# Kernel tuning notes

Hardware: AMD Instinct MI355X
Metric: run time of the kernel (lower is better)

Reference implementation:

```python
import jax, jax.numpy as jnp
import numpy as np

N_NODES = 20000
N_EDGES = 320000
N_FEAT = 128
HID = 64
HEADS = 4
N_CLS = 16
NEG_SLOPE = 0.2


def setup_inputs() -> dict:
    key = jax.random.key(0)
    ks = jax.random.split(key, 12)
    x = jax.random.normal(ks[0], (N_NODES, N_FEAT), dtype=jnp.float32)
    edge_index = jax.random.randint(ks[1], (2, N_EDGES), 0, N_NODES, dtype=jnp.int64)
    # layer 1: GATConv(128 -> 64, heads=4, concat)
    s1 = 1.0 / np.sqrt(N_FEAT)
    W1 = jax.random.uniform(ks[2], (N_FEAT, HEADS * HID), jnp.float32, -s1, s1)
    a_src1 = jax.random.uniform(ks[3], (HEADS, HID), jnp.float32, -s1, s1)
    a_dst1 = jax.random.uniform(ks[4], (HEADS, HID), jnp.float32, -s1, s1)
    b1 = jnp.zeros((HEADS * HID,), jnp.float32)
    # layer 2: GATConv(256 -> 16, heads=1)
    s2 = 1.0 / np.sqrt(HEADS * HID)
    W2 = jax.random.uniform(ks[5], (HEADS * HID, N_CLS), jnp.float32, -s2, s2)
    a_src2 = jax.random.uniform(ks[6], (1, N_CLS), jnp.float32, -s2, s2)
    a_dst2 = jax.random.uniform(ks[7], (1, N_CLS), jnp.float32, -s2, s2)
    b2 = jnp.zeros((N_CLS,), jnp.float32)
    return {"x": x, "edge_index": edge_index, "W1": W1, "a_src1": a_src1,
            "a_dst1": a_dst1, "b1": b1, "W2": W2, "a_src2": a_src2,
            "a_dst2": a_dst2, "b2": b2}


def gat_conv(x, src, dst, W, a_src, a_dst, bias, n_nodes):
    # x: [N, F_in]; W: [F_in, H*C]; a_src/a_dst: [H, C]
    H, C = a_src.shape
    h = (x @ W).reshape(n_nodes, H, C)                     # [N, H, C]
    al_src = jnp.sum(h * a_src[None], axis=-1)             # [N, H]
    al_dst = jnp.sum(h * a_dst[None], axis=-1)             # [N, H]
    e = jax.nn.leaky_relu(al_src[src] + al_dst[dst], NEG_SLOPE)  # [E, H]
    # segment softmax over incoming edges of each destination node
    m = jax.ops.segment_max(e, dst, num_segments=n_nodes)  # [N, H]
    e = jnp.exp(e - m[dst])
    denom = jax.ops.segment_sum(e, dst, num_segments=n_nodes)
    alpha = e / (denom[dst] + 1e-16)                       # [E, H]
    msg = h[src] * alpha[:, :, None]                       # [E, H, C]
    out = jax.ops.segment_sum(msg, dst, num_segments=n_nodes)  # [N, H, C]
    return out.reshape(n_nodes, H * C) + bias


def reference(x, edge_index, W1, a_src1, a_dst1, b1, W2, a_src2, a_dst2, b2):
    n = x.shape[0]
    loops = jnp.arange(n, dtype=edge_index.dtype)
    src = jnp.concatenate([edge_index[0], loops])
    dst = jnp.concatenate([edge_index[1], loops])
    # eval mode: dropout is identity
    h = jax.nn.elu(gat_conv(x, src, dst, W1, a_src1, a_dst1, b1, n))
    out = gat_conv(h, src, dst, W2, a_src2, a_dst2, b2, n)
    return out
```

## Files before the change

### kernel.cpp

```cpp
#include <hip/hip_runtime.h>
#include <hip/hip_bf16.h>
#include <hip/hip_fp16.h>
#include <math.h>

#define N_NODES 20000
#define N_EDGES 320000
#define E_TOT   (N_EDGES + N_NODES)
#define N_FEAT  128
#define NEG_SLOPE 0.2f
#define MAXDEG  96

typedef _Float16 half8 __attribute__((ext_vector_type(8)));
typedef float f32x4 __attribute__((ext_vector_type(4)));

__global__ void k_init(int* __restrict__ cur,
                       const float* __restrict__ x, _Float16* __restrict__ xh,
                       const float* __restrict__ W1, _Float16* __restrict__ W1t){
  int tid = blockIdx.x * blockDim.x + threadIdx.x;
  if (tid < N_NODES) cur[tid] = 0;
  if (tid < (N_NODES * N_FEAT / 8)){
    float4 a = *(const float4*)&x[(size_t)tid * 8];
    float4 b = *(const float4*)&x[(size_t)tid * 8 + 4];
    union { __half2 h2[4]; half8 h8; } u;
    u.h2[0] = __floats2half2_rn(a.x, a.y);
    u.h2[1] = __floats2half2_rn(a.z, a.w);
    u.h2[2] = __floats2half2_rn(b.x, b.y);
    u.h2[3] = __floats2half2_rn(b.z, b.w);
    *(half8*)&xh[(size_t)tid * 8] = u.h8;
  }
  if (tid < 4096){
    int n = tid >> 4, ks = tid & 15;
    union { __half2 h2[4]; half8 h8; } u;
    float v[8];
    #pragma unroll
    for (int r = 0; r < 8; ++r) v[r] = W1[(size_t)(ks * 8 + r) * 256 + n];
    u.h2[0] = __floats2half2_rn(v[0], v[1]);
    u.h2[1] = __floats2half2_rn(v[2], v[3]);
    u.h2[2] = __floats2half2_rn(v[4], v[5]);
    u.h2[3] = __floats2half2_rn(v[6], v[7]);
    *(half8*)&W1t[(size_t)n * 128 + ks * 8] = u.h8;
  }
}

__global__ __launch_bounds__(256) void k_gemm1(
                        const _Float16* __restrict__ xh, const _Float16* __restrict__ W1t,
                        const float* __restrict__ as1, const float* __restrict__ ad1,
                        _Float16* __restrict__ h1h,
                        float* __restrict__ alS, float* __restrict__ alD,
                        const int* __restrict__ ei, int* __restrict__ cur,
                        int* __restrict__ adjS){
  __shared__ _Float16 xt[64][136];
  __shared__ _Float16 Wt[64][136];
  int t  = threadIdx.x;

  {
    int fb = blockIdx.y * 313 + blockIdx.x;
    int gtid = fb * 256 + t;
    const int GSZ = 313 * 4 * 256;
    for (int e = gtid; e < E_TOT; e += GSZ){
      int s, d;
      if (e < N_EDGES){ s = ei[e]; d = ei[N_EDGES + e]; }
      else            { s = d = e - N_EDGES; }
      int pos = atomicAdd(&cur[d], 1);
      if (pos < MAXDEG) adjS[d * MAXDEG + pos] = s;
    }
  }

  int m0 = blockIdx.x * 64;
  int by = blockIdx.y;
  int j0 = by * 64;
  #pragma unroll
  for (int ii = 0; ii < 4; ++ii){
    int f = t + ii * 256;
    int r = f >> 4, s = f & 15;
    half8 xv = (half8)(_Float16)0.f;
    if (m0 + r < N_NODES) xv = *(const half8*)&xh[(size_t)(m0 + r) * 128 + s * 8];
    *(half8*)&xt[r][s * 8] = xv;
    half8 wv = *(const half8*)&W1t[(size_t)(j0 + r) * 128 + s * 8];
    *(half8*)&Wt[r][s * 8] = wv;
  }
  __syncthreads();

  int w = t >> 6, lane = t & 63;
  int g = lane >> 4, mi = lane & 15;
  f32x4 acc[4] = {};
  #pragma unroll
  for (int kk = 0; kk < 4; ++kk){
    int ko = kk * 32 + g * 8;
    half8 b = *(const half8*)&xt[w * 16 + mi][ko];
    #pragma unroll
    for (int s = 0; s < 4; ++s){
      half8 a = *(const half8*)&Wt[s * 16 + mi][ko];
      acc[s] = __builtin_amdgcn_mfma_f32_16x16x32_f16(a, b, acc[s], 0, 0, 0);
    }
  }

  int m = m0 + w * 16 + mi;
  float s_ = 0.f, d_ = 0.f;
  #pragma unroll
  for (int s = 0; s < 4; ++s){
    int nb = j0 + s * 16 + g * 4;
    float4 asv = *(const float4*)&as1[nb];
    float4 adv = *(const float4*)&ad1[nb];
    s_ += acc[s][0] * asv.x + acc[s][1] * asv.y + acc[s][2] * asv.z + acc[s][3] * asv.w;
    d_ += acc[s][0] * adv.x + acc[s][1] * adv.y + acc[s][2] * adv.z + acc[s][3] * adv.w;
    if (m < N_NODES){
      union { __half2 h2[2]; float2 f2; } u;
      u.h2[0] = __floats2half2_rn(acc[s][0], acc[s][1]);
      u.h2[1] = __floats2half2_rn(acc[s][2], acc[s][3]);
      *(float2*)&h1h[(size_t)m * 256 + nb] = u.f2;
    }
  }
  s_ += __shfl_xor(s_, 16); s_ += __shfl_xor(s_, 32);
  d_ += __shfl_xor(d_, 16); d_ += __shfl_xor(d_, 32);
  if (g == 0 && m < N_NODES){ alS[m * 4 + by] = s_; alD[m * 4 + by] = d_; }
}

__global__ __launch_bounds__(256) void k_attn1(
                        const int* __restrict__ cur, const int* __restrict__ adjS,
                        const __half* __restrict__ h1h,
                        const float* __restrict__ alS, const float* __restrict__ alD,
                        const float* __restrict__ b1, _Float16* __restrict__ heluh){
  int b    = blockIdx.x;
  int slot = b & 7;
  int h    = slot & 3;
  int g    = (slot >> 2) * 625 + (b >> 3);
  int t    = threadIdx.x;
  int w    = t >> 6, lane = t & 63;
  int grp  = lane >> 4, l16 = lane & 15;
  int n    = g * 16 + w * 4 + grp;

  int cnt  = cur[n]; cnt = (cnt > MAXDEG) ? MAXDEG : cnt;
  int start = n * MAXDEG, end = start + cnt;
  float ald = alD[n * 4 + h];
  const __half* __restrict__ hb = h1h + h * 64 + l16 * 4;

  float4 A0 = make_float4(0.f,0.f,0.f,0.f), A1 = A0, A2 = A0, A3 = A0;
  float d0 = 0.f, d1 = 0.f, d2 = 0.f, d3 = 0.f;
  int i = start;
  if (i + 3 < end){
    int4 q = *(const int4*)&adjS[i];
    while (i + 3 < end){
      int s0 = q.x, s1 = q.y, s2 = q.z, s3 = q.w;
      int inext = i + 4;
      if (inext + 3 < end) q = *(const int4*)&adjS[inext];
      float t0 = alS[s0 * 4 + h] + ald;
      float t1 = alS[s1 * 4 + h] + ald;
      float t2 = alS[s2 * 4 + h] + ald;
      float t3 = alS[s3 * 4 + h] + ald;
      t0 = (t0 > 0.f) ? t0 : NEG_SLOPE * t0;
      t1 = (t1 > 0.f) ? t1 : NEG_SLOPE * t1;
      t2 = (t2 > 0.f) ? t2 : NEG_SLOPE * t2;
      t3 = (t3 > 0.f) ? t3 : NEG_SLOPE * t3;
      float w0 = __expf(t0), w1 = __expf(t1), w2 = __expf(t2), w3 = __expf(t3);
      float2 r0 = *(const float2*)&hb[(size_t)s0 * 256];
      float2 r1 = *(const float2*)&hb[(size_t)s1 * 256];
      float2 r2 = *(const float2*)&hb[(size_t)s2 * 256];
      float2 r3 = *(const float2*)&hb[(size_t)s3 * 256];
      const __half2* p0 = (const __half2*)&r0;
      const __half2* p1 = (const __half2*)&r1;
      const __half2* p2 = (const __half2*)&r2;
      const __half2* p3 = (const __half2*)&r3;
      float2 v0a = __half22float2(p0[0]), v0b = __half22float2(p0[1]);
      float2 v1a = __half22float2(p1[0]), v1b = __half22float2(p1[1]);
      float2 v2a = __half22float2(p2[0]), v2b = __half22float2(p2[1]);
      float2 v3a = __half22float2(p3[0]), v3b = __half22float2(p3[1]);
      A0.x += w0 * v0a.x; A0.y += w0 * v0a.y; A0.z += w0 * v0b.x; A0.w += w0 * v0b.y;
      A1.x += w1 * v1a.x; A1.y += w1 * v1a.y; A1.z += w1 * v1b.x; A1.w += w1 * v1b.y;
      A2.x += w2 * v2a.x; A2.y += w2 * v2a.y; A2.z += w2 * v2b.x; A2.w += w2 * v2b.y;
      A3.x += w3 * v3a.x; A3.y += w3 * v3a.y; A3.z += w3 * v3b.x; A3.w += w3 * v3b.y;
      d0 += w0; d1 += w1; d2 += w2; d3 += w3;
      i = inext;
    }
  }
  for (; i < end; ++i){
    int s0 = adjS[i];
    float t0 = alS[s0 * 4 + h] + ald;
    t0 = (t0 > 0.f) ? t0 : NEG_SLOPE * t0;
    float w0 = __expf(t0);
    float2 r0 = *(const float2*)&hb[(size_t)s0 * 256];
    const __half2* p0 = (const __half2*)&r0;
    float2 v0a = __half22float2(p0[0]), v0b = __half22float2(p0[1]);
    A0.x += w0 * v0a.x; A0.y += w0 * v0a.y; A0.z += w0 * v0b.x; A0.w += w0 * v0b.y;
    d0 += w0;
  }
  float rinv = 1.f / (((d0 + d1) + (d2 + d3)) + 1e-16f);
  float4 bv = *(const float4*)&b1[h * 64 + l16 * 4];
  float4 o;
  o.x = ((A0.x + A1.x) + (A2.x + A3.x)) * rinv + bv.x;
  o.y = ((A0.y + A1.y) + (A2.y + A3.y)) * rinv + bv.y;
  o.z = ((A0.z + A1.z) + (A2.z + A3.z)) * rinv + bv.z;
  o.w = ((A0.w + A1.w) + (A2.w + A3.w)) * rinv + bv.w;
  o.x = (o.x > 0.f) ? o.x : (__expf(o.x) - 1.f);
  o.y = (o.y > 0.f) ? o.y : (__expf(o.y) - 1.f);
  o.z = (o.z > 0.f) ? o.z : (__expf(o.z) - 1.f);
  o.w = (o.w > 0.f) ? o.w : (__expf(o.w) - 1.f);
  union { __half2 h2[2]; float2 f2; } u;
  u.h2[0] = __floats2half2_rn(o.x, o.y);
  u.h2[1] = __floats2half2_rn(o.z, o.w);
  *(float2*)&heluh[(size_t)n * 256 + h * 64 + l16 * 4] = u.f2;
}

__global__ __launch_bounds__(256) void k_gemm2(
                        const _Float16* __restrict__ heluh, const float* __restrict__ W2,
                        const float* __restrict__ as2, const float* __restrict__ ad2,
                        float* __restrict__ h2, float* __restrict__ alS, float* __restrict__ alD){
  __shared__ _Float16 Ht[64][264];
  __shared__ _Float16 Wt[16][264];
  int t = threadIdx.x;
  int n0 = blockIdx.x * 64;
  #pragma unroll
  for (int ii = 0; ii < 8; ++ii){
    int f = t + ii * 256;
    int r = f >> 5, s = f & 31;
    half8 v = (half8)(_Float16)0.f;
    if (n0 + r < N_NODES) v = *(const half8*)&heluh[(size_t)(n0 + r) * 256 + s * 8];
    *(half8*)&Ht[r][s * 8] = v;
  }
  {
    int k = t;
    float4 w0 = *(const float4*)&W2[k * 16 + 0];
    float4 w1 = *(const float4*)&W2[k * 16 + 4];
    float4 w2 = *(const float4*)&W2[k * 16 + 8];
    float4 w3 = *(const float4*)&W2[k * 16 + 12];
    float wv[16] = {w0.x,w0.y,w0.z,w0.w, w1.x,w1.y,w1.z,w1.w,
                    w2.x,w2.y,w2.z,w2.w, w3.x,w3.y,w3.z,w3.w};
    #pragma unroll
    for (int c = 0; c < 16; ++c) Wt[c][k] = (_Float16)wv[c];
  }
  __syncthreads();

  int w = t >> 6, lane = t & 63;
  int g = lane >> 4, mi = lane & 15;
  f32x4 acc = {};
  #pragma unroll
  for (int kk = 0; kk < 8; ++kk){
    int ko = kk * 32 + g * 8;
    half8 b = *(const half8*)&Ht[w * 16 + mi][ko];
    half8 a = *(const half8*)&Wt[mi][ko];
    acc = __builtin_amdgcn_mfma_f32_16x16x32_f16(a, b, acc, 0, 0, 0);
  }
  int n = n0 + w * 16 + mi;
  float4 asv = *(const float4*)&as2[g * 4];
  float4 adv = *(const float4*)&ad2[g * 4];
  float s_ = acc[0] * asv.x + acc[1] * asv.y + acc[2] * asv.z + acc[3] * asv.w;
  float d_ = acc[0] * adv.x + acc[1] * adv.y + acc[2] * adv.z + acc[3] * adv.w;
  s_ += __shfl_xor(s_, 16); s_ += __shfl_xor(s_, 32);
  d_ += __shfl_xor(d_, 16); d_ += __shfl_xor(d_, 32);
  if (n < N_NODES){
    float4 hv = make_float4(acc[0], acc[1], acc[2], acc[3]);
    *(float4*)&h2[(size_t)n * 16 + g * 4] = hv;
    if (g == 0){ alS[n] = s_; alD[n] = d_; }
  }
}

__global__ __launch_bounds__(256) void k_attn2(
                        const int* __restrict__ cur, const int* __restrict__ adjS,
                        const float* __restrict__ h2,
                        const float* __restrict__ alS, const float* __restrict__ alD,
                        const float* __restrict__ b2, float* __restrict__ out){
  int t    = threadIdx.x;
  int w    = t >> 6, lane = t & 63;
  int grp  = lane >> 4, l16 = lane & 15;
  int j    = l16 >> 2, c4 = l16 & 3;
  int n    = blockIdx.x * 16 + w * 4 + grp;

  int cnt  = cur[n]; cnt = (cnt > MAXDEG) ? MAXDEG : cnt;
  int start = n * MAXDEG, end = start + cnt;
  float ald = alD[n];
  float4 acc = make_float4(0.f,0.f,0.f,0.f);
  float den = 0.f;
  for (int i = start + j; i < end; i += 4){
    int s = adjS[i];
    float tt = alS[s] + ald;
    tt = (tt > 0.f) ? tt : NEG_SLOPE * tt;
    float wv = __expf(tt);
    float4 v = *(const float4*)&h2[(size_t)s * 16 + c4 * 4];
    acc.x += wv * v.x; acc.y += wv * v.y; acc.z += wv * v.z; acc.w += wv * v.w;
    den += wv;
  }
  #pragma unroll
  for (int off = 4; off <= 8; off <<= 1){
    acc.x += __shfl_xor(acc.x, off);
    acc.y += __shfl_xor(acc.y, off);
    acc.z += __shfl_xor(acc.z, off);
    acc.w += __shfl_xor(acc.w, off);
    den   += __shfl_xor(den, off);
  }
  if (j == 0){
    float rinv = 1.f / (den + 1e-16f);
    float4 bv = *(const float4*)&b2[c4 * 4];
    float4 o;
    o.x = acc.x * rinv + bv.x; o.y = acc.y * rinv + bv.y;
    o.z = acc.z * rinv + bv.z; o.w = acc.w * rinv + bv.w;
    *(float4*)&out[(size_t)n * 16 + c4 * 4] = o;
  }
}

extern "C" void kernel_launch(void* const* d_in, const int* in_sizes, int n_in,
                              void* d_out, int out_size, void* d_ws, size_t ws_size,
                              hipStream_t stream){
  const float* x   = (const float*)d_in[0];
  const int*   ei  = (const int*)d_in[1];
  const float* W1  = (const float*)d_in[2];
  const float* as1 = (const float*)d_in[3];
  const float* ad1 = (const float*)d_in[4];
  const float* b1  = (const float*)d_in[5];
  const float* W2  = (const float*)d_in[6];
  const float* as2 = (const float*)d_in[7];
  const float* ad2 = (const float*)d_in[8];
  const float* b2  = (const float*)d_in[9];
  float* out = (float*)d_out;

  float* fws = (float*)d_ws;
  size_t off = 0;
  __half* h1h = (__half*)(fws + off); off += (size_t)N_NODES * 128;
  _Float16* xh  = (_Float16*)(fws + off); off += (size_t)N_NODES * 64;
  _Float16* W1t = (_Float16*)(fws + off); off += 256 * 64;
  _Float16* heluh = (_Float16*)(fws + off); off += (size_t)N_NODES * 128;
  float* h2   = fws + off; off += (size_t)N_NODES * 16;
  float* alS1 = fws + off; off += N_NODES * 4;
  float* alD1 = fws + off; off += N_NODES * 4;
  float* alS2 = fws + off; off += N_NODES;
  float* alD2 = fws + off; off += N_NODES;
  int* cur  = (int*)(fws + off); off += N_NODES;
  int* adjS = (int*)(fws + off); off += (size_t)N_NODES * MAXDEG;

  k_init<<<(N_NODES * N_FEAT / 8 + 255) / 256, 256, 0, stream>>>(cur, x, xh, W1, W1t);
  k_gemm1<<<dim3(313, 4), 256, 0, stream>>>(xh, W1t, as1, ad1, (_Float16*)h1h,
                                            alS1, alD1, ei, cur, adjS);
  k_attn1<<<5000, 256, 0, stream>>>(cur, adjS, h1h, alS1, alD1, b1, heluh);
  k_gemm2<<<313, 256, 0, stream>>>(heluh, W2, as2, ad2, h2, alS2, alD2);
  k_attn2<<<1250, 256, 0, stream>>>(cur, adjS, h2, alS2, alD2, b2, out);
}
```

Before: 80.15 us.

## Fuse x fp16 conversion into gemm1 and split neighbor loop across half-groups

Converts x to fp16 directly while loading gemm1 tiles, removing the separate xh buffer and its write/read pass in k_init. In k_attn1, each 16-lane node group is split into two halves that process alternating quads of neighbors with 8-feature 16-byte loads, then combine partial sums via a lane shuffle. This aims to shorten the serial gather chain per lane and widen loads, at the cost of extra shuffles and half the lanes idle during the final write.

```diff
diff --git a/kernel.cpp b/kernel.cpp
--- a/kernel.cpp
+++ b/kernel.cpp
@@ -14,20 +14,9 @@
 typedef float f32x4 __attribute__((ext_vector_type(4)));
 
 __global__ void k_init(int* __restrict__ cur,
-                       const float* __restrict__ x, _Float16* __restrict__ xh,
                        const float* __restrict__ W1, _Float16* __restrict__ W1t){
   int tid = blockIdx.x * blockDim.x + threadIdx.x;
   if (tid < N_NODES) cur[tid] = 0;
-  if (tid < (N_NODES * N_FEAT / 8)){
-    float4 a = *(const float4*)&x[(size_t)tid * 8];
-    float4 b = *(const float4*)&x[(size_t)tid * 8 + 4];
-    union { __half2 h2[4]; half8 h8; } u;
-    u.h2[0] = __floats2half2_rn(a.x, a.y);
-    u.h2[1] = __floats2half2_rn(a.z, a.w);
-    u.h2[2] = __floats2half2_rn(b.x, b.y);
-    u.h2[3] = __floats2half2_rn(b.z, b.w);
-    *(half8*)&xh[(size_t)tid * 8] = u.h8;
-  }
   if (tid < 4096){
     int n = tid >> 4, ks = tid & 15;
     union { __half2 h2[4]; half8 h8; } u;
@@ -43,7 +32,7 @@
 }
 
 __global__ __launch_bounds__(256) void k_gemm1(
-                        const _Float16* __restrict__ xh, const _Float16* __restrict__ W1t,
+                        const float* __restrict__ x, const _Float16* __restrict__ W1t,
                         const float* __restrict__ as1, const float* __restrict__ ad1,
                         _Float16* __restrict__ h1h,
                         float* __restrict__ alS, float* __restrict__ alD,
@@ -74,7 +63,16 @@
     int f = t + ii * 256;
     int r = f >> 4, s = f & 15;
     half8 xv = (half8)(_Float16)0.f;
-    if (m0 + r < N_NODES) xv = *(const half8*)&xh[(size_t)(m0 + r) * 128 + s * 8];
+    if (m0 + r < N_NODES){
+      float4 a = *(const float4*)&x[(size_t)(m0 + r) * 128 + s * 8];
+      float4 bq = *(const float4*)&x[(size_t)(m0 + r) * 128 + s * 8 + 4];
+      union { __half2 h2[4]; half8 h8; } u;
+      u.h2[0] = __floats2half2_rn(a.x, a.y);
+      u.h2[1] = __floats2half2_rn(a.z, a.w);
+      u.h2[2] = __floats2half2_rn(bq.x, bq.y);
+      u.h2[3] = __floats2half2_rn(bq.z, bq.w);
+      xv = u.h8;
+    }
     *(half8*)&xt[r][s * 8] = xv;
     half8 wv = *(const half8*)&W1t[(size_t)(j0 + r) * 128 + s * 8];
     *(half8*)&Wt[r][s * 8] = wv;
@@ -128,77 +126,112 @@
   int t    = threadIdx.x;
   int w    = t >> 6, lane = t & 63;
   int grp  = lane >> 4, l16 = lane & 15;
+  int hf   = l16 >> 3, l8 = l16 & 7;
   int n    = g * 16 + w * 4 + grp;
 
   int cnt  = cur[n]; cnt = (cnt > MAXDEG) ? MAXDEG : cnt;
-  int start = n * MAXDEG, end = start + cnt;
+  int base = n * MAXDEG;
   float ald = alD[n * 4 + h];
-  const __half* __restrict__ hb = h1h + h * 64 + l16 * 4;
-
-  float4 A0 = make_float4(0.f,0.f,0.f,0.f), A1 = A0, A2 = A0, A3 = A0;
-  float d0 = 0.f, d1 = 0.f, d2 = 0.f, d3 = 0.f;
-  int i = start;
-  if (i + 3 < end){
-    int4 q = *(const int4*)&adjS[i];
-    while (i + 3 < end){
-      int s0 = q.x, s1 = q.y, s2 = q.z, s3 = q.w;
-      int inext = i + 4;
-      if (inext + 3 < end) q = *(const int4*)&adjS[inext];
+  const __half* __restrict__ hb = h1h + h * 64 + l8 * 8;
+
+  float4 Aa = make_float4(0.f,0.f,0.f,0.f), Ab = Aa;
+  float den = 0.f;
+
+  int nq = cnt >> 2;
+  for (int q = hf; q < nq; q += 2){
+    int4 quad = *(const int4*)&adjS[base + q * 4];
+    int s0 = quad.x, s1 = quad.y, s2 = quad.z, s3 = quad.w;
+    float t0 = alS[s0 * 4 + h] + ald;
+    float t1 = alS[s1 * 4 + h] + ald;
+    float t2 = alS[s2 * 4 + h] + ald;
+    float t3 = alS[s3 * 4 + h] + ald;
+    t0 = (t0 > 0.f) ? t0 : NEG_SLOPE * t0;
+    t1 = (t1 > 0.f) ? t1 : NEG_SLOPE * t1;
+    t2 = (t2 > 0.f) ? t2 : NEG_SLOPE * t2;
+    t3 = (t3 > 0.f) ? t3 : NEG_SLOPE * t3;
+    float w0 = __expf(t0), w1 = __expf(t1), w2 = __expf(t2), w3 = __expf(t3);
+    float4 r0 = *(const float4*)&hb[(size_t)s0 * 256];
+    float4 r1 = *(const float4*)&hb[(size_t)s1 * 256];
+    float4 r2 = *(const float4*)&hb[(size_t)s2 * 256];
+    float4 r3 = *(const float4*)&hb[(size_t)s3 * 256];
+    const __half2* p0 = (const __half2*)&r0;
+    const __half2* p1 = (const __half2*)&r1;
+    const __half2* p2 = (const __half2*)&r2;
+    const __half2* p3 = (const __half2*)&r3;
+    {
+      float2 a0 = __half22float2(p0[0]), a1 = __half22float2(p0[1]);
+      float2 a2 = __half22float2(p0[2]), a3 = __half22float2(p0[3]);
+      Aa.x += w0 * a0.x; Aa.y += w0 * a0.y; Aa.z += w0 * a1.x; Aa.w += w0 * a1.y;
+      Ab.x += w0 * a2.x; Ab.y += w0 * a2.y; Ab.z += w0 * a3.x; Ab.w += w0 * a3.y;
+    }
+    {
+      float2 a0 = __half22float2(p1[0]), a1 = __half22float2(p1[1]);
+      float2 a2 = __half22float2(p1[2]), a3 = __half22float2(p1[3]);
+      Aa.x += w1 * a0.x; Aa.y += w1 * a0.y; Aa.z += w1 * a1.x; Aa.w += w1 * a1.y;
+      Ab.x += w1 * a2.x; Ab.y += w1 * a2.y; Ab.z += w1 * a3.x; Ab.w += w1 * a3.y;
+    }
+    {
+      float2 a0 = __half22float2(p2[0]), a1 = __half22float2(p2[1]);
+      float2 a2 = __half22float2(p2[2]), a3 = __half22float2(p2[3]);
+      Aa.x += w2 * a0.x; Aa.y += w2 * a0.y; Aa.z += w2 * a1.x; Aa.w += w2 * a1.y;
+      Ab.x += w2 * a2.x; Ab.y += w2 * a2.y; Ab.z += w2 * a3.x; Ab.w += w2 * a3.y;
+    }
+    {
+      float2 a0 = __half22float2(p3[0]), a1 = __half22float2(p3[1]);
+      float2 a2 = __half22float2(p3[2]), a3 = __half22float2(p3[3]);
+      Aa.x += w3 * a0.x; Aa.y += w3 * a0.y; Aa.z += w3 * a1.x; Aa.w += w3 * a1.y;
+      Ab.x += w3 * a2.x; Ab.y += w3 * a2.y; Ab.z += w3 * a3.x; Ab.w += w3 * a3.y;
+    }
+    den += ((w0 + w1) + (w2 + w3));
+  }
+  if ((nq & 1) == hf){
+    for (int i = base + nq * 4; i < base + cnt; ++i){
+      int s0 = adjS[i];
       float t0 = alS[s0 * 4 + h] + ald;
-      float t1 = alS[s1 * 4 + h] + ald;
-      float t2 = alS[s2 * 4 + h] + ald;
-      float t3 = alS[s3 * 4 + h] + ald;
       t0 = (t0 > 0.f) ? t0 : NEG_SLOPE * t0;
-      t1 = (t1 > 0.f) ? t1 : NEG_SLOPE * t1;
-      t2 = (t2 > 0.f) ? t2 : NEG_SLOPE * t2;
-      t3 = (t3 > 0.f) ? t3 : NEG_SLOPE * t3;
-      float w0 = __expf(t0), w1 = __expf(t1), w2 = __expf(t2), w3 = __expf(t3);
-      float2 r0 = *(const float2*)&hb[(size_t)s0 * 256];
-      float2 r1 = *(const float2*)&hb[(size_t)s1 * 256];
-      float2 r2 = *(const float2*)&hb[(size_t)s2 * 256];
-      float2 r3 = *(const float2*)&hb[(size_t)s3 * 256];
+      float w0 = __expf(t0);
+      float4 r0 = *(const float4*)&hb[(size_t)s0 * 256];
       const __half2* p0 = (const __half2*)&r0;
-      const __half2* p1 = (const __half2*)&r1;
-      const __half2* p2 = (const __half2*)&r2;
-      const __half2* p3 = (const __half2*)&r3;
-      float2 v0a = __half22float2(p0[0]), v0b = __half22float2(p0[1]);
-      float2 v1a = __half22float2(p1[0]), v1b = __half22float2(p1[1]);
-      float2 v2a = __half22float2(p2[0]), v2b = __half22float2(p2[1]);
-      float2 v3a = __half22float2(p3[0]), v3b = __half22float2(p3[1]);
-      A0.x += w0 * v0a.x; A0.y += w0 * v0a.y; A0.z += w0 * v0b.x; A0.w += w0 * v0b.y;
-      A1.x += w1 * v1a.x; A1.y += w1 * v1a.y; A1.z += w1 * v1b.x; A1.w += w1 * v1b.y;
-      A2.x += w2 * v2a.x; A2.y += w2 * v2a.y; A2.z += w2 * v2b.x; A2.w += w2 * v2b.y;
-      A3.x += w3 * v3a.x; A3.y += w3 * v3a.y; A3.z += w3 * v3b.x; A3.w += w3 * v3b.y;
-      d0 += w0; d1 += w1; d2 += w2; d3 += w3;
-      i = inext;
-    }
-  }
-  for (; i < end; ++i){
-    int s0 = adjS[i];
-    float t0 = alS[s0 * 4 + h] + ald;
-    t0 = (t0 > 0.f) ? t0 : NEG_SLOPE * t0;
-    float w0 = __expf(t0);
-    float2 r0 = *(const float2*)&hb[(size_t)s0 * 256];
-    const __half2* p0 = (const __half2*)&r0;
-    float2 v0a = __half22float2(p0[0]), v0b = __half22float2(p0[1]);
-    A0.x += w0 * v0a.x; A0.y += w0 * v0a.y; A0.z += w0 * v0b.x; A0.w += w0 * v0b.y;
-    d0 += w0;
-  }
-  float rinv = 1.f / (((d0 + d1) + (d2 + d3)) + 1e-16f);
-  float4 bv = *(const float4*)&b1[h * 64 + l16 * 4];
-  float4 o;
-  o.x = ((A0.x + A1.x) + (A2.x + A3.x)) * rinv + bv.x;
-  o.y = ((A0.y + A1.y) + (A2.y + A3.y)) * rinv + bv.y;
-  o.z = ((A0.z + A1.z) + (A2.z + A3.z)) * rinv + bv.z;
-  o.w = ((A0.w + A1.w) + (A2.w + A3.w)) * rinv + bv.w;
-  o.x = (o.x > 0.f) ? o.x : (__expf(o.x) - 1.f);
-  o.y = (o.y > 0.f) ? o.y : (__expf(o.y) - 1.f);
-  o.z = (o.z > 0.f) ? o.z : (__expf(o.z) - 1.f);
-  o.w = (o.w > 0.f) ? o.w : (__expf(o.w) - 1.f);
-  union { __half2 h2[2]; float2 f2; } u;
-  u.h2[0] = __floats2half2_rn(o.x, o.y);
-  u.h2[1] = __floats2half2_rn(o.z, o.w);
-  *(float2*)&heluh[(size_t)n * 256 + h * 64 + l16 * 4] = u.f2;
+      float2 a0 = __half22float2(p0[0]), a1 = __half22float2(p0[1]);
+      float2 a2 = __half22float2(p0[2]), a3 = __half22float2(p0[3]);
+      Aa.x += w0 * a0.x; Aa.y += w0 * a0.y; Aa.z += w0 * a1.x; Aa.w += w0 * a1.y;
+      Ab.x += w0 * a2.x; Ab.y += w0 * a2.y; Ab.z += w0 * a3.x; Ab.w += w0 * a3.y;
+      den += w0;
+    }
+  }
+  Aa.x += __shfl_xor(Aa.x, 8); Aa.y += __shfl_xor(Aa.y, 8);
+  Aa.z += __shfl_xor(Aa.z, 8); Aa.w += __shfl_xor(Aa.w, 8);
+  Ab.x += __shfl_xor(Ab.x, 8); Ab.y += __shfl_xor(Ab.y, 8);
+  Ab.z += __shfl_xor(Ab.z, 8); Ab.w += __shfl_xor(Ab.w, 8);
+  den  += __shfl_xor(den, 8);
+
+  if (hf == 0){
+    float rinv = 1.f / (den + 1e-16f);
+    float4 bv0 = *(const float4*)&b1[h * 64 + l8 * 8];
+    float4 bv1 = *(const float4*)&b1[h * 64 + l8 * 8 + 4];
+    float o0 = Aa.x * rinv + bv0.x;
+    float o1 = Aa.y * rinv + bv0.y;
+    float o2 = Aa.z * rinv + bv0.z;
+    float o3 = Aa.w * rinv + bv0.w;
+    float o4 = Ab.x * rinv + bv1.x;
+    float o5 = Ab.y * rinv + bv1.y;
+    float o6 = Ab.z * rinv + bv1.z;
+    float o7 = Ab.w * rinv + bv1.w;
+    o0 = (o0 > 0.f) ? o0 : (__expf(o0) - 1.f);
+    o1 = (o1 > 0.f) ? o1 : (__expf(o1) - 1.f);
+    o2 = (o2 > 0.f) ? o2 : (__expf(o2) - 1.f);
+    o3 = (o3 > 0.f) ? o3 : (__expf(o3) - 1.f);
+    o4 = (o4 > 0.f) ? o4 : (__expf(o4) - 1.f);
+    o5 = (o5 > 0.f) ? o5 : (__expf(o5) - 1.f);
+    o6 = (o6 > 0.f) ? o6 : (__expf(o6) - 1.f);
+    o7 = (o7 > 0.f) ? o7 : (__expf(o7) - 1.f);
+    union { __half2 h2[4]; half8 h8; } u;
+    u.h2[0] = __floats2half2_rn(o0, o1);
+    u.h2[1] = __floats2half2_rn(o2, o3);
+    u.h2[2] = __floats2half2_rn(o4, o5);
+    u.h2[3] = __floats2half2_rn(o6, o7);
+    *(half8*)&heluh[(size_t)n * 256 + h * 64 + l8 * 8] = u.h8;
+  }
 }
 
 __global__ __launch_bounds__(256) void k_gemm2(
@@ -315,7 +348,6 @@
   float* fws = (float*)d_ws;
   size_t off = 0;
   __half* h1h = (__half*)(fws + off); off += (size_t)N_NODES * 128;
-  _Float16* xh  = (_Float16*)(fws + off); off += (size_t)N_NODES * 64;
   _Float16* W1t = (_Float16*)(fws + off); off += 256 * 64;
   _Float16* heluh = (_Float16*)(fws + off); off += (size_t)N_NODES * 128;
   float* h2   = fws + off; off += (size_t)N_NODES * 16;
@@ -326,8 +358,8 @@
   int* cur  = (int*)(fws + off); off += N_NODES;
   int* adjS = (int*)(fws + off); off += (size_t)N_NODES * MAXDEG;
 
-  k_init<<<(N_NODES * N_FEAT / 8 + 255) / 256, 256, 0, stream>>>(cur, x, xh, W1, W1t);
-  k_gemm1<<<dim3(313, 4), 256, 0, stream>>>(xh, W1t, as1, ad1, (_Float16*)h1h,
+  k_init<<<(N_NODES + 255) / 256, 256, 0, stream>>>(cur, W1, W1t);
+  k_gemm1<<<dim3(313, 4), 256, 0, stream>>>(x, W1t, as1, ad1, (_Float16*)h1h,
                                             alS1, alD1, ei, cur, adjS);
   k_attn1<<<5000, 256, 0, stream>>>(cur, adjS, h1h, alS1, alD1, b1, heluh);
   k_gemm2<<<313, 256, 0, stream>>>(heluh, W2, as2, ad2, h2, alS2, alD2);
```

New measurement: 78.22 us. -2.4%, faster.
